# Optimization experiments

Measured on AMD Instinct MI355X. Metric: run time of the kernel, lower is better.

## Reference

```python
import jax, jax.numpy as jnp
import numpy as np

N_HEAD = 16
ROPE_BASE = 10000.0

def _rotate_half(x):
    # matches torch: stack((-x[...,1::2], x[...,::2]), -1).flatten(-2)
    x1 = x[..., ::2]
    x2 = x[..., 1::2]
    return jnp.stack((-x2, x1), axis=-1).reshape(x.shape)

def setup_inputs() -> dict:
    key = jax.random.key(0)
    ks = jax.random.split(key, 5)
    B, T, C = 4, 2048, 1024
    x = jax.random.normal(ks[0], (B, T, C), dtype=jnp.float32)
    Wq = jax.random.normal(ks[1], (C, C), dtype=jnp.float32) * 0.02
    Wk = jax.random.normal(ks[2], (C, C), dtype=jnp.float32) * 0.02
    Wv = jax.random.normal(ks[3], (C, C), dtype=jnp.float32) * 0.02
    Wp = jax.random.normal(ks[4], (C, C), dtype=jnp.float32) * 0.02
    return {"x": x, "Wq": Wq, "Wk": Wk, "Wv": Wv, "Wp": Wp, "start_pos": 0}

def reference(x, Wq, Wk, Wv, Wp, start_pos):
    B, T, C = x.shape
    H = N_HEAD
    D = C // H
    # torch Linear: out = x @ W^T
    q = jnp.einsum('btc,dc->btd', x, Wq).reshape(B, T, H, D).transpose(0, 2, 1, 3)
    k = jnp.einsum('btc,dc->btd', x, Wk).reshape(B, T, H, D).transpose(0, 2, 1, 3)
    v = jnp.einsum('btc,dc->btd', x, Wv).reshape(B, T, H, D).transpose(0, 2, 1, 3)
    # RoPE cache (cat[freqs, freqs] with interleaved rotate_half, as in source)
    inv_freq = 1.0 / (ROPE_BASE ** (jnp.arange(0, D, 2, dtype=jnp.float32) / D))
    t = jnp.arange(T, dtype=jnp.float32) + jnp.float32(start_pos)
    freqs = t[:, None] * inv_freq[None, :]          # [T, D/2]
    emb = jnp.concatenate([freqs, freqs], axis=-1)  # [T, D]
    cos = jnp.cos(emb)[None, None]                  # [1,1,T,D]
    sin = jnp.sin(emb)[None, None]
    q = q * cos + _rotate_half(q) * sin
    k = k * cos + _rotate_half(k) * sin
    att = jnp.einsum('bhqd,bhkd->bhqk', q, k) / jnp.sqrt(jnp.float32(D))
    mask = jnp.triu(jnp.ones((T, T), dtype=bool), k=1)
    att = jnp.where(mask, -jnp.inf, att)
    att = jax.nn.softmax(att, axis=-1)
    y = jnp.einsum('bhqk,bhkd->bhqd', att, v)
    y = y.transpose(0, 2, 1, 3).reshape(B, T, C)
    return jnp.einsum('btc,dc->btd', y, Wp)
```

## Files before the change

kernel.cpp:

```cpp
#include <hip/hip_runtime.h>
#include <hip/hip_bf16.h>
#include <stdint.h>

#define B_  4
#define T_  2048
#define C_  1024
#define H_  16
#define D_  64
#define BT  (B_*T_)
#define KDIM 1024

typedef __attribute__((ext_vector_type(8))) short bf16x8;
typedef __attribute__((ext_vector_type(4))) float f32x4;

__device__ __forceinline__ unsigned short f2bf(float f) {
  union { float f; unsigned u; } v; v.f = f;
  unsigned r = v.u + 0x7FFFu + ((v.u >> 16) & 1u);
  return (unsigned short)(r >> 16);
}

__device__ __forceinline__ float exp2_fast(float x) {
  float r;
  asm("v_exp_f32 %0, %1" : "=v"(r) : "v"(x));
  return r;
}

__device__ __forceinline__ void gld_lds16(const void* g, void* l) {
  __builtin_amdgcn_global_load_lds(
      (__attribute__((address_space(1))) unsigned int*)(uintptr_t)g,
      (__attribute__((address_space(3))) unsigned int*)(unsigned)(uintptr_t)l,
      16, 0, 0);
}

__global__ __launch_bounds__(256) void k_convert(
    const float* __restrict__ x,  const float* __restrict__ wq,
    const float* __restrict__ wk, const float* __restrict__ wv,
    const float* __restrict__ wp,
    unsigned short* __restrict__ xb, unsigned short* __restrict__ wcat,
    unsigned short* __restrict__ wpb)
{
  const int NX = BT*C_/4;
  const int NW = C_*C_/4;
  const int TOT = NX + 4*NW;
  for (int i = blockIdx.x*blockDim.x + threadIdx.x; i < TOT; i += gridDim.x*blockDim.x) {
    const float4* src; unsigned short* dst; int idx;
    if (i < NX)                { src = (const float4*)x;  dst = xb;            idx = i; }
    else {
      int j = i - NX;
      if (j < NW)              { src = (const float4*)wq; dst = wcat;          idx = j; }
      else if (j < 2*NW)       { src = (const float4*)wk; dst = wcat + C_*C_;  idx = j - NW; }
      else if (j < 3*NW)       { src = (const float4*)wv; dst = wcat + 2*C_*C_;idx = j - 2*NW; }
      else                     { src = (const float4*)wp; dst = wpb;           idx = j - 3*NW; }
    }
    float4 v = src[idx];
    ushort4 o; o.x = f2bf(v.x); o.y = f2bf(v.y); o.z = f2bf(v.z); o.w = f2bf(v.w);
    *(ushort4*)(dst + (size_t)idx*4) = o;
  }
}

__global__ __launch_bounds__(256) void k_rope_tab(
    const int* __restrict__ start_pos, float* __restrict__ cosT, float* __restrict__ sinT)
{
  int i = blockIdx.x*blockDim.x + threadIdx.x;
  if (i >= T_*D_) return;
  int t = i >> 6, j = i & 63;
  float inv = exp2f(-(float)(j & 31) * (13.287712379549449f / 32.0f));
  float ang = (float)(t + start_pos[0]) * inv;
  cosT[i] = cosf(ang);
  sinT[i] = sinf(ang);
}

__global__ __launch_bounds__(512, 2) void k_gemm256(
    const unsigned short* __restrict__ A, const unsigned short* __restrict__ Bw,
    unsigned short* __restrict__ qb, unsigned short* __restrict__ kb,
    unsigned short* __restrict__ vt,
    const float* __restrict__ cosT, const float* __restrict__ sinT)
{
  __shared__ __attribute__((aligned(16))) char smem[131072];
  const int tid = threadIdx.x, l = tid & 63, w = tid >> 6;
  const int g = l >> 4, c = l & 15;
  const int m0 = blockIdx.x * 256, n0 = blockIdx.y * 256;
  const int wr = w >> 2, wc = w & 3;
  const char* gA = (const char*)A;
  const char* gB = (const char*)Bw;

  int dstU[2]; size_t aoff[2], boff[2];
#pragma unroll
  for (int j = 0; j < 2; ++j) {
    int P = j*8192 + tid*16;
    int p = P >> 7;
    int inner = (P & 127) ^ ((p & 7) << 4);
    int row = (p << 1) | (inner >> 6);
    int kc = (inner & 63) >> 1;
    dstU[j] = P;
    aoff[j] = ((size_t)(m0 + row) * KDIM + kc) * 2;
    boff[j] = ((size_t)(n0 + row) * KDIM + kc) * 2;
  }

  const int swzo = ((((c & 1) << 6) | (g << 4)) ^ (((c >> 1) & 7) << 4));
  const int aB = (wr*64 + (c >> 1)) * 128 + swzo;
  const int bB = 32768 + (wc*32 + (c >> 1)) * 128 + swzo;

  f32x4 acc[8][4];
#pragma unroll
  for (int i = 0; i < 8; ++i)
#pragma unroll
    for (int j = 0; j < 4; ++j) acc[i][j] = (f32x4){0.f,0.f,0.f,0.f};

#pragma unroll
  for (int j = 0; j < 2; ++j) gld_lds16(gA + aoff[j],      smem +     0 + dstU[j]);
#pragma unroll
  for (int j = 0; j < 2; ++j) gld_lds16(gB + boff[j],      smem + 32768 + dstU[j]);
#pragma unroll
  for (int j = 0; j < 2; ++j) gld_lds16(gA + aoff[j] + 64, smem + 16384 + dstU[j]);
#pragma unroll
  for (int j = 0; j < 2; ++j) gld_lds16(gB + boff[j] + 64, smem + 49152 + dstU[j]);
  asm volatile("s_waitcnt vmcnt(4)" ::: "memory");
  __builtin_amdgcn_s_barrier();

#define MFMA16(MB)                                                               \
    __builtin_amdgcn_s_setprio(1);                                               \
    _Pragma("unroll")                                                            \
    for (int i2 = 0; i2 < 4; ++i2)                                               \
      _Pragma("unroll")                                                          \
      for (int ni = 0; ni < 4; ++ni)                                             \
        acc[(MB)+i2][ni] = __builtin_amdgcn_mfma_f32_16x16x32_bf16(              \
            af[i2], bk[ni], acc[(MB)+i2][ni], 0, 0, 0);                          \
    __builtin_amdgcn_s_setprio(0);

#define PRE_MFMA                                                                 \
    __builtin_amdgcn_s_barrier();                                                \
    asm volatile("s_waitcnt lgkmcnt(0)" ::: "memory");                           \
    __builtin_amdgcn_sched_barrier(0);

  bf16x8 af[4], bk[4];

#pragma unroll 2
  for (int t = 0; t < 15; ++t) {
    const int par = (t & 1) << 16;
    const int nxt = par ^ 65536;
    const size_t ko = (size_t)(t + 1) * 128;

#pragma unroll
    for (int i2 = 0; i2 < 4; ++i2) af[i2] = *(const bf16x8*)(smem + par + aB + i2*1024);
#pragma unroll
    for (int ni = 0; ni < 4; ++ni) bk[ni] = *(const bf16x8*)(smem + par + bB + ni*1024);
#pragma unroll
    for (int j = 0; j < 2; ++j) gld_lds16(gA + aoff[j] + ko, smem + nxt + dstU[j]);
    PRE_MFMA
    MFMA16(0)
    __builtin_amdgcn_s_barrier();

#pragma unroll
    for (int i2 = 0; i2 < 4; ++i2) af[i2] = *(const bf16x8*)(smem + par + aB + (4+i2)*1024);
#pragma unroll
    for (int j = 0; j < 2; ++j) gld_lds16(gB + boff[j] + ko, smem + nxt + 32768 + dstU[j]);
    PRE_MFMA
    MFMA16(4)
    asm volatile("s_waitcnt vmcnt(4)" ::: "memory");
    __builtin_amdgcn_s_barrier();

#pragma unroll
    for (int i2 = 0; i2 < 4; ++i2) af[i2] = *(const bf16x8*)(smem + par + 16384 + aB + i2*1024);
#pragma unroll
    for (int ni = 0; ni < 4; ++ni) bk[ni] = *(const bf16x8*)(smem + par + 16384 + bB + ni*1024);
#pragma unroll
    for (int j = 0; j < 2; ++j) gld_lds16(gA + aoff[j] + ko + 64, smem + nxt + 16384 + dstU[j]);
    PRE_MFMA
    MFMA16(0)
    __builtin_amdgcn_s_barrier();

#pragma unroll
    for (int i2 = 0; i2 < 4; ++i2) af[i2] = *(const bf16x8*)(smem + par + 16384 + aB + (4+i2)*1024);
#pragma unroll
    for (int j = 0; j < 2; ++j) gld_lds16(gB + boff[j] + ko + 64, smem + nxt + 49152 + dstU[j]);
    PRE_MFMA
    MFMA16(4)
    asm volatile("s_waitcnt vmcnt(4)" ::: "memory");
    __builtin_amdgcn_s_barrier();
  }

  {
    const int par = 65536;
#pragma unroll
    for (int i2 = 0; i2 < 4; ++i2) af[i2] = *(const bf16x8*)(smem + par + aB + i2*1024);
#pragma unroll
    for (int ni = 0; ni < 4; ++ni) bk[ni] = *(const bf16x8*)(smem + par + bB + ni*1024);
    PRE_MFMA
    MFMA16(0)
    __builtin_amdgcn_s_barrier();
#pragma unroll
    for (int i2 = 0; i2 < 4; ++i2) af[i2] = *(const bf16x8*)(smem + par + aB + (4+i2)*1024);
    PRE_MFMA
    MFMA16(4)
    asm volatile("s_waitcnt vmcnt(0)" ::: "memory");
    __builtin_amdgcn_s_barrier();
#pragma unroll
    for (int i2 = 0; i2 < 4; ++i2) af[i2] = *(const bf16x8*)(smem + par + 16384 + aB + i2*1024);
#pragma unroll
    for (int ni = 0; ni < 4; ++ni) bk[ni] = *(const bf16x8*)(smem + par + 16384 + bB + ni*1024);
    PRE_MFMA
    MFMA16(0)
    __builtin_amdgcn_s_barrier();
#pragma unroll
    for (int i2 = 0; i2 < 4; ++i2) af[i2] = *(const bf16x8*)(smem + par + 16384 + aB + (4+i2)*1024);
    PRE_MFMA
    MFMA16(4)
  }
#undef MFMA16
#undef PRE_MFMA

#pragma unroll
  for (int mi = 0; mi < 8; ++mi) {
#pragma unroll
    for (int ni = 0; ni < 4; ++ni) {
      const int mrow0 = m0 + wr*128 + mi*16 + g*4;
      const int ncol  = n0 + wc*64 + ni*16 + c;
      const int which = ncol >> 10;
      const int d = ncol & 1023, h = d >> 6, dd = d & 63;
      const int b = mrow0 >> 11, t0 = mrow0 & 2047;
      if (which == 2) {
        ushort4 o;
        o.x = f2bf(acc[mi][ni][0]); o.y = f2bf(acc[mi][ni][1]);
        o.z = f2bf(acc[mi][ni][2]); o.w = f2bf(acc[mi][ni][3]);
        *(ushort4*)(vt + ((size_t)((b*H_ + h)*D_ + dd))*T_ + t0) = o;
      } else {
#pragma unroll
        for (int r = 0; r < 4; ++r) {
          float val = acc[mi][ni][r];
          float partner = __shfl_xor(val, 1);
          float rot = (dd & 1) ? partner : -partner;
          float cv = cosT[(t0 + r)*64 + dd], sv = sinT[(t0 + r)*64 + dd];
          float o = val*cv + rot*sv;
          size_t oidx = (((size_t)(b*H_ + h))*T_ + (t0 + r))*D_ + dd;
          if (which == 0) qb[oidx] = f2bf(o * 0.180336879f);
          else            kb[oidx] = f2bf(o);
        }
      }
    }
  }
}

template<int EPI>
__global__ __launch_bounds__(256) void k_gemm(
    const unsigned short* __restrict__ A, const unsigned short* __restrict__ Bw,
    unsigned short* __restrict__ qb, unsigned short* __restrict__ kb,
    unsigned short* __restrict__ vt,
    const float* __restrict__ cosT, const float* __restrict__ sinT,
    float* __restrict__ outF)
{
  __shared__ __attribute__((aligned(16))) char smem[32768];
  const int tid = threadIdx.x, l = tid & 63, w = tid >> 6;
  const int g = l >> 4, c = l & 15;
  const int m0 = blockIdx.x * 128, n0 = blockIdx.y * 128;
  const int wr = w >> 1, wc = w & 1;

  const char* srcA[4]; const char* srcB[4]; int dstP[4];
#pragma unroll
  for (int j = 0; j < 4; ++j) {
    int P = w*4096 + j*1024 + l*16;
    int row = P >> 7;
    int Lb = P ^ ((row & 7) << 4);
    int col = (Lb & 127) >> 1;
    dstP[j] = P;
    srcA[j] = (const char*)A  + ((size_t)(m0 + row) * KDIM + col) * 2;
    srcB[j] = (const char*)Bw + ((size_t)(n0 + row) * KDIM + col) * 2;
  }

  f32x4 acc[4][4];
#pragma unroll
  for (int i = 0; i < 4; ++i)
#pragma unroll
    for (int j = 0; j < 4; ++j) acc[i][j] = (f32x4){0.f,0.f,0.f,0.f};

  for (int kt = 0; kt < KDIM; kt += 64) {
#pragma unroll
    for (int j = 0; j < 4; ++j) {
      gld_lds16(srcA[j] + kt*2, smem + dstP[j]);
      gld_lds16(srcB[j] + kt*2, smem + 16384 + dstP[j]);
    }
    __syncthreads();
#pragma unroll
    for (int kk = 0; kk < 2; ++kk) {
      bf16x8 af[4], bw4[4];
#pragma unroll
      for (int mi = 0; mi < 4; ++mi) {
        int row = wr*64 + mi*16 + c;
        int Lb = row*128 + (kk*32 + g*8)*2;
        af[mi] = *(const bf16x8*)(smem + (Lb ^ ((row & 7) << 4)));
      }
#pragma unroll
      for (int ni = 0; ni < 4; ++ni) {
        int row = wc*64 + ni*16 + c;
        int Lb = row*128 + (kk*32 + g*8)*2;
        bw4[ni] = *(const bf16x8*)(smem + 16384 + (Lb ^ ((row & 7) << 4)));
      }
#pragma unroll
      for (int mi = 0; mi < 4; ++mi)
#pragma unroll
        for (int ni = 0; ni < 4; ++ni)
          acc[mi][ni] = __builtin_amdgcn_mfma_f32_16x16x32_bf16(af[mi], bw4[ni], acc[mi][ni], 0, 0, 0);
    }
    __syncthreads();
  }

#pragma unroll
  for (int mi = 0; mi < 4; ++mi) {
#pragma unroll
    for (int ni = 0; ni < 4; ++ni) {
      const int mrow0 = m0 + wr*64 + mi*16 + g*4;
      const int ncol  = n0 + wc*64 + ni*16 + c;
      if (EPI == 1) {
#pragma unroll
        for (int r = 0; r < 4; ++r)
          outF[(size_t)(mrow0 + r) * 1024 + ncol] = acc[mi][ni][r];
      } else {
        const int which = ncol >> 10;
        const int d = ncol & 1023, h = d >> 6, dd = d & 63;
        const int b = mrow0 >> 11, t0 = mrow0 & 2047;
        if (which == 2) {
          ushort4 o;
          o.x = f2bf(acc[mi][ni][0]); o.y = f2bf(acc[mi][ni][1]);
          o.z = f2bf(acc[mi][ni][2]); o.w = f2bf(acc[mi][ni][3]);
          *(ushort4*)(vt + ((size_t)((b*H_ + h)*D_ + dd))*T_ + t0) = o;
        } else {
#pragma unroll
          for (int r = 0; r < 4; ++r) {
            float val = acc[mi][ni][r];
            float partner = __shfl_xor(val, 1);
            float rot = (dd & 1) ? partner : -partner;
            float cv = cosT[(t0 + r)*64 + dd], sv = sinT[(t0 + r)*64 + dd];
            float o = val*cv + rot*sv;
            size_t oidx = (((size_t)(b*H_ + h))*T_ + (t0 + r))*D_ + dd;
            if (which == 0) qb[oidx] = f2bf(o * 0.180336879f);
            else            kb[oidx] = f2bf(o);
          }
        }
      }
    }
  }
}

__global__ __launch_bounds__(512) void k_attn(
    const unsigned short* __restrict__ qb, const unsigned short* __restrict__ kb,
    const unsigned short* __restrict__ vt, unsigned short* __restrict__ yb)
{
  __shared__ __attribute__((aligned(16))) char smem[65536];
  const int tid = threadIdx.x, l = tid & 63, w = tid >> 6;
  const int g = l >> 4, c = l & 15;
  const int bh = blockIdx.x;
  const int pidx = blockIdx.y;
  const size_t bhO = (size_t)bh * T_ * D_;
  const int pbase = 49152 + w*2048;
  const int b = bh >> 4, h = bh & 15;

  bf16x8 vones;
#pragma unroll
  for (int i = 0; i < 8; ++i) vones[i] = (short)0x3F80;

  const char* srcK; const char* srcV; int dstP2;
  {
    int P = w*1024 + l*16;
    int row = P >> 7;
    int Lb = P ^ ((row & 7) << 4);
    int col = (Lb & 127) >> 1;
    dstP2 = P;
    srcK = (const char*)(kb + bhO) + ((size_t)row*D_ + col)*2;
    srcV = (const char*)(vt + bhO) + ((size_t)row*T_ + col)*2;
  }

  for (int half = 0; half < 2; ++half) {
    const int qt = half ? pidx : (15 - pidx);
    const int q0 = qt * 128;
    const int q0w = q0 + w*16;

    bf16x8 aq[2];
#pragma unroll
    for (int kc = 0; kc < 2; ++kc)
      aq[kc] = *(const bf16x8*)(qb + bhO + (size_t)(q0w + c)*D_ + kc*32 + g*8);

    f32x4 po[4];
    f32x4 ls;
    float mrun = -1e30f;
#pragma unroll
    for (int nd = 0; nd < 4; ++nd) po[nd] = (f32x4){0.f,0.f,0.f,0.f};
    ls = (f32x4){0.f,0.f,0.f,0.f};

    const int nkt = (q0 + 128) >> 6;

    gld_lds16(srcK, smem + dstP2);
    gld_lds16(srcV, smem + 8192 + dstP2);
    gld_lds16(srcK + (size_t)64*128, smem + 16384 + dstP2);
    gld_lds16(srcV + (size_t)64*2,   smem + 16384 + 8192 + dstP2);
    asm volatile("s_waitcnt vmcnt(2)" ::: "memory");
    __builtin_amdgcn_s_barrier();
    __builtin_amdgcn_sched_barrier(0);

    int rd = 0;
    for (int it = 0; it < nkt; ++it) {
      const int kv0 = it * 64;
      const int cur = rd * 16384;

      if (it + 2 < nkt) {
        int wi = rd + 2; if (wi >= 3) wi -= 3;
        const int wb = wi * 16384;
        gld_lds16(srcK + (size_t)(kv0 + 128) * 128, smem + wb + dstP2);
        gld_lds16(srcV + (size_t)(kv0 + 128) * 2,   smem + wb + 8192 + dstP2);
      }

      if (kv0 < q0w + 16) {
        f32x4 st[4];
#pragma unroll
        for (int ni = 0; ni < 4; ++ni) st[ni] = (f32x4){0.f,0.f,0.f,0.f};
        __builtin_amdgcn_s_setprio(1);
#pragma unroll
        for (int kk = 0; kk < 2; ++kk) {
          bf16x8 bk[4];
#pragma unroll
          for (int ni = 0; ni < 4; ++ni) {
            int kn = ni*16 + c;
            int Lb = kn*128 + (kk*32 + g*8)*2;
            bk[ni] = *(const bf16x8*)(smem + cur + (Lb ^ ((kn & 7) << 4)));
          }
#pragma unroll
          for (int ni = 0; ni < 4; ++ni)
            st[ni] = __builtin_amdgcn_mfma_f32_16x16x32_bf16(bk[ni], aq[kk], st[ni], 0, 0, 0);
        }
        __builtin_amdgcn_s_setprio(0);

        if (kv0 + 64 > q0w) {
          const int qq = q0w + c;
#pragma unroll
          for (int ni = 0; ni < 4; ++ni)
#pragma unroll
            for (int r = 0; r < 4; ++r) {
              int kvv = kv0 + ni*16 + g*4 + r;
              if (kvv > qq) st[ni][r] = -1e30f;
            }
        }

        {
          float mn[4];
#pragma unroll
          for (int ni = 0; ni < 4; ++ni)
            mn[ni] = fmaxf(fmaxf(st[ni][0], st[ni][1]), fmaxf(st[ni][2], st[ni][3]));
          float mt = fmaxf(fmaxf(mn[0], mn[1]), fmaxf(mn[2], mn[3]));
          mt = fmaxf(mt, __shfl_xor(mt, 16));
          mt = fmaxf(mt, __shfl_xor(mt, 32));
          float m_use = mrun;
          if (__any(mt > m_use + 8.f)) {
            float mnew = fmaxf(m_use, mt);
            float alpha = exp2_fast(m_use - mnew);
            mrun = mnew;
            m_use = mnew;
#pragma unroll
            for (int r = 0; r < 4; ++r) ls[r] *= alpha;
#pragma unroll
            for (int nd = 0; nd < 4; ++nd)
#pragma unroll
              for (int r = 0; r < 4; ++r) po[nd][r] *= alpha;
          }
#pragma unroll
          for (int ni = 0; ni < 4; ++ni)
#pragma unroll
            for (int r = 0; r < 4; ++r)
              st[ni][r] = exp2_fast(st[ni][r] - m_use);
        }

        {
          const int row = c;
          const int sw = (row & 7) << 4;
          const int rb = pbase + row*128;
#pragma unroll
          for (int ni = 0; ni < 4; ++ni) {
            unsigned u0, u1;
            asm("v_cvt_pk_bf16_f32 %0, %1, %2" : "=v"(u0) : "v"(st[ni][0]), "v"(st[ni][1]));
            asm("v_cvt_pk_bf16_f32 %0, %1, %2" : "=v"(u1) : "v"(st[ni][2]), "v"(st[ni][3]));
            int Lb = (ni*16 + g*4) * 2;
            uint2 uu; uu.x = u0; uu.y = u1;
            *(uint2*)(smem + rb + (Lb ^ sw)) = uu;
          }
        }

        __builtin_amdgcn_s_setprio(1);
#pragma unroll
        for (int kk = 0; kk < 2; ++kk) {
          bf16x8 pb;
          {
            int pr = c;
            int Lb = pr*128 + (kk*32 + g*8)*2;
            pb = *(const bf16x8*)(smem + pbase + (Lb ^ ((pr & 7) << 4)));
          }
          ls = __builtin_amdgcn_mfma_f32_16x16x32_bf16(vones, pb, ls, 0, 0, 0);
          bf16x8 bv[4];
#pragma unroll
          for (int nd = 0; nd < 4; ++nd) {
            int vr = nd*16 + c;
            int Lb = vr*128 + (kk*32 + g*8)*2;
            bv[nd] = *(const bf16x8*)(smem + cur + 8192 + (Lb ^ ((vr & 7) << 4)));
          }
#pragma unroll
          for (int nd = 0; nd < 4; ++nd)
            po[nd] = __builtin_amdgcn_mfma_f32_16x16x32_bf16(bv[nd], pb, po[nd], 0, 0, 0);
        }
        __builtin_amdgcn_s_setprio(0);
      }

      if (it + 1 < nkt) {
        if (it + 2 < nkt) { asm volatile("s_waitcnt vmcnt(2)" ::: "memory"); }
        else              { asm volatile("s_waitcnt vmcnt(0)" ::: "memory"); }
      }
      __builtin_amdgcn_s_barrier();
      __builtin_amdgcn_sched_barrier(0);
      rd = (rd == 2) ? 0 : rd + 1;
    }

    {
      float inv = 1.f / ls[0];
      int t = q0w + c;
#pragma unroll
      for (int nd = 0; nd < 4; ++nd) {
        ushort4 o;
        o.x = f2bf(po[nd][0] * inv);
        o.y = f2bf(po[nd][1] * inv);
        o.z = f2bf(po[nd][2] * inv);
        o.w = f2bf(po[nd][3] * inv);
        *(ushort4*)(yb + ((size_t)b*T_ + t)*C_ + h*64 + nd*16 + g*4) = o;
      }
    }
  }
}

extern "C" void kernel_launch(void* const* d_in, const int* in_sizes, int n_in,
                              void* d_out, int out_size, void* d_ws, size_t ws_size,
                              hipStream_t stream)
{
  const float* x  = (const float*)d_in[0];
  const float* Wq = (const float*)d_in[1];
  const float* Wk = (const float*)d_in[2];
  const float* Wv = (const float*)d_in[3];
  const float* Wp = (const float*)d_in[4];
  const int*   sp = (const int*)d_in[5];
  float* out = (float*)d_out;

  char* ws = (char*)d_ws;
  unsigned short* xb   = (unsigned short*)(ws);
  unsigned short* wcat = (unsigned short*)(ws + 16777216);
  unsigned short* wpb  = (unsigned short*)(ws + 23068672);
  unsigned short* qb   = (unsigned short*)(ws + 25165824);
  unsigned short* kb   = (unsigned short*)(ws + 41943040);
  unsigned short* vt   = (unsigned short*)(ws + 58720256);
  unsigned short* yb   = (unsigned short*)(ws + 75497472);
  float* cosT = (float*)(ws + 92274688);
  float* sinT = (float*)(ws + 92798976);

  k_convert<<<dim3(2048), dim3(256), 0, stream>>>(x, Wq, Wk, Wv, Wp, xb, wcat, wpb);
  k_rope_tab<<<dim3(512), dim3(256), 0, stream>>>(sp, cosT, sinT);
  k_gemm256<<<dim3(32, 12), dim3(512), 0, stream>>>(xb, wcat, qb, kb, vt, cosT, sinT);
  k_attn<<<dim3(64, 8), dim3(512), 0, stream>>>(qb, kb, vt, yb);
  k_gemm<1><<<dim3(64, 8), dim3(256), 0, stream>>>(yb, wpb, nullptr, nullptr, nullptr, nullptr, nullptr, out);
}
```

Measured before the change: 173.4 us.

## Simplify QKV GEMM main loop to full-tile double buffering with XOR-swizzled rows

Result: faster. 168.8 us (-2.6%).

```diff
diff --git a/kernel.cpp b/kernel.cpp
--- a/kernel.cpp
+++ b/kernel.cpp
@@ -84,22 +84,20 @@
   const char* gA = (const char*)A;
   const char* gB = (const char*)Bw;
 
-  int dstU[2]; size_t aoff[2], boff[2];
-#pragma unroll
-  for (int j = 0; j < 2; ++j) {
+  int dstP[4]; size_t aoff[4], boff[4];
+#pragma unroll
+  for (int j = 0; j < 4; ++j) {
     int P = j*8192 + tid*16;
-    int p = P >> 7;
-    int inner = (P & 127) ^ ((p & 7) << 4);
-    int row = (p << 1) | (inner >> 6);
-    int kc = (inner & 63) >> 1;
-    dstU[j] = P;
+    int row = P >> 7;
+    int kc = ((P & 127) ^ ((row & 7) << 4)) >> 1;
+    dstP[j] = P;
     aoff[j] = ((size_t)(m0 + row) * KDIM + kc) * 2;
     boff[j] = ((size_t)(n0 + row) * KDIM + kc) * 2;
   }
 
-  const int swzo = ((((c & 1) << 6) | (g << 4)) ^ (((c >> 1) & 7) << 4));
-  const int aB = (wr*64 + (c >> 1)) * 128 + swzo;
-  const int bB = 32768 + (wc*32 + (c >> 1)) * 128 + swzo;
+  const int aBase = (wr*128 + c) * 128;
+  const int bBase = 32768 + (wc*64 + c) * 128;
+  const int xsw = (c & 7) << 4;
 
   f32x4 acc[8][4];
 #pragma unroll
@@ -108,107 +106,45 @@
     for (int j = 0; j < 4; ++j) acc[i][j] = (f32x4){0.f,0.f,0.f,0.f};
 
 #pragma unroll
-  for (int j = 0; j < 2; ++j) gld_lds16(gA + aoff[j],      smem +     0 + dstU[j]);
-#pragma unroll
-  for (int j = 0; j < 2; ++j) gld_lds16(gB + boff[j],      smem + 32768 + dstU[j]);
-#pragma unroll
-  for (int j = 0; j < 2; ++j) gld_lds16(gA + aoff[j] + 64, smem + 16384 + dstU[j]);
-#pragma unroll
-  for (int j = 0; j < 2; ++j) gld_lds16(gB + boff[j] + 64, smem + 49152 + dstU[j]);
-  asm volatile("s_waitcnt vmcnt(4)" ::: "memory");
-  __builtin_amdgcn_s_barrier();
-
-#define MFMA16(MB)                                                               \
-    __builtin_amdgcn_s_setprio(1);                                               \
-    _Pragma("unroll")                                                            \
-    for (int i2 = 0; i2 < 4; ++i2)                                               \
-      _Pragma("unroll")                                                          \
-      for (int ni = 0; ni < 4; ++ni)                                             \
-        acc[(MB)+i2][ni] = __builtin_amdgcn_mfma_f32_16x16x32_bf16(              \
-            af[i2], bk[ni], acc[(MB)+i2][ni], 0, 0, 0);                          \
-    __builtin_amdgcn_s_setprio(0);
-
-#define PRE_MFMA                                                                 \
-    __builtin_amdgcn_s_barrier();                                                \
-    asm volatile("s_waitcnt lgkmcnt(0)" ::: "memory");                           \
-    __builtin_amdgcn_sched_barrier(0);
-
-  bf16x8 af[4], bk[4];
-
-#pragma unroll 2
-  for (int t = 0; t < 15; ++t) {
+  for (int j = 0; j < 4; ++j) {
+    gld_lds16(gA + aoff[j], smem + dstP[j]);
+    gld_lds16(gB + boff[j], smem + 32768 + dstP[j]);
+  }
+
+  for (int t = 0; t < 16; ++t) {
     const int par = (t & 1) << 16;
     const int nxt = par ^ 65536;
-    const size_t ko = (size_t)(t + 1) * 128;
-
-#pragma unroll
-    for (int i2 = 0; i2 < 4; ++i2) af[i2] = *(const bf16x8*)(smem + par + aB + i2*1024);
-#pragma unroll
-    for (int ni = 0; ni < 4; ++ni) bk[ni] = *(const bf16x8*)(smem + par + bB + ni*1024);
-#pragma unroll
-    for (int j = 0; j < 2; ++j) gld_lds16(gA + aoff[j] + ko, smem + nxt + dstU[j]);
-    PRE_MFMA
-    MFMA16(0)
-    __builtin_amdgcn_s_barrier();
-
-#pragma unroll
-    for (int i2 = 0; i2 < 4; ++i2) af[i2] = *(const bf16x8*)(smem + par + aB + (4+i2)*1024);
-#pragma unroll
-    for (int j = 0; j < 2; ++j) gld_lds16(gB + boff[j] + ko, smem + nxt + 32768 + dstU[j]);
-    PRE_MFMA
-    MFMA16(4)
-    asm volatile("s_waitcnt vmcnt(4)" ::: "memory");
-    __builtin_amdgcn_s_barrier();
-
-#pragma unroll
-    for (int i2 = 0; i2 < 4; ++i2) af[i2] = *(const bf16x8*)(smem + par + 16384 + aB + i2*1024);
-#pragma unroll
-    for (int ni = 0; ni < 4; ++ni) bk[ni] = *(const bf16x8*)(smem + par + 16384 + bB + ni*1024);
-#pragma unroll
-    for (int j = 0; j < 2; ++j) gld_lds16(gA + aoff[j] + ko + 64, smem + nxt + 16384 + dstU[j]);
-    PRE_MFMA
-    MFMA16(0)
-    __builtin_amdgcn_s_barrier();
-
-#pragma unroll
-    for (int i2 = 0; i2 < 4; ++i2) af[i2] = *(const bf16x8*)(smem + par + 16384 + aB + (4+i2)*1024);
-#pragma unroll
-    for (int j = 0; j < 2; ++j) gld_lds16(gB + boff[j] + ko + 64, smem + nxt + 49152 + dstU[j]);
-    PRE_MFMA
-    MFMA16(4)
-    asm volatile("s_waitcnt vmcnt(4)" ::: "memory");
-    __builtin_amdgcn_s_barrier();
-  }
-
-  {
-    const int par = 65536;
-#pragma unroll
-    for (int i2 = 0; i2 < 4; ++i2) af[i2] = *(const bf16x8*)(smem + par + aB + i2*1024);
-#pragma unroll
-    for (int ni = 0; ni < 4; ++ni) bk[ni] = *(const bf16x8*)(smem + par + bB + ni*1024);
-    PRE_MFMA
-    MFMA16(0)
-    __builtin_amdgcn_s_barrier();
-#pragma unroll
-    for (int i2 = 0; i2 < 4; ++i2) af[i2] = *(const bf16x8*)(smem + par + aB + (4+i2)*1024);
-    PRE_MFMA
-    MFMA16(4)
-    asm volatile("s_waitcnt vmcnt(0)" ::: "memory");
-    __builtin_amdgcn_s_barrier();
-#pragma unroll
-    for (int i2 = 0; i2 < 4; ++i2) af[i2] = *(const bf16x8*)(smem + par + 16384 + aB + i2*1024);
-#pragma unroll
-    for (int ni = 0; ni < 4; ++ni) bk[ni] = *(const bf16x8*)(smem + par + 16384 + bB + ni*1024);
-    PRE_MFMA
-    MFMA16(0)
-    __builtin_amdgcn_s_barrier();
-#pragma unroll
-    for (int i2 = 0; i2 < 4; ++i2) af[i2] = *(const bf16x8*)(smem + par + 16384 + aB + (4+i2)*1024);
-    PRE_MFMA
-    MFMA16(4)
-  }
-#undef MFMA16
-#undef PRE_MFMA
+
+    __syncthreads();
+
+    if (t + 1 < 16) {
+      const size_t ko = (size_t)(t + 1) * 128;
+#pragma unroll
+      for (int j = 0; j < 4; ++j) {
+        gld_lds16(gA + aoff[j] + ko, smem + nxt + dstP[j]);
+        gld_lds16(gB + boff[j] + ko, smem + nxt + 32768 + dstP[j]);
+      }
+    }
+
+#pragma unroll
+    for (int kk = 0; kk < 2; ++kk) {
+      const int xt = (kk*64 + g*16) ^ xsw;
+      bf16x8 bk[4], af[8];
+#pragma unroll
+      for (int ni = 0; ni < 4; ++ni)
+        bk[ni] = *(const bf16x8*)(smem + par + bBase + ni*2048 + xt);
+#pragma unroll
+      for (int mi = 0; mi < 8; ++mi)
+        af[mi] = *(const bf16x8*)(smem + par + aBase + mi*2048 + xt);
+      __builtin_amdgcn_s_setprio(1);
+#pragma unroll
+      for (int mi = 0; mi < 8; ++mi)
+#pragma unroll
+        for (int ni = 0; ni < 4; ++ni)
+          acc[mi][ni] = __builtin_amdgcn_mfma_f32_16x16x32_bf16(af[mi], bk[ni], acc[mi][ni], 0, 0, 0);
+      __builtin_amdgcn_s_setprio(0);
+    }
+  }
 
 #pragma unroll
   for (int mi = 0; mi < 8; ++mi) {
```
